# Kernel optimization log

Hardware: AMD Instinct MI355X
Metric: run time of the kernel (lower is better)

The kernel has to match this reference:

```python
import jax, jax.numpy as jnp
import numpy as np

EPS = 1e-5
H, W, C, NCLS = 8, 16, 64, 8

def _bn_params(key, c):
    k1, k2, k3, k4 = jax.random.split(key, 4)
    gamma = jax.random.uniform(k1, (c,), minval=0.5, maxval=1.5)
    beta = 0.1 * jax.random.normal(k2, (c,))
    mean = 0.1 * jax.random.normal(k3, (c,))
    var = jax.random.uniform(k4, (c,), minval=0.5, maxval=1.5)
    return jnp.stack([gamma, beta, mean, var]).astype(jnp.float32)  # (4, c)

def bn2d(x, p):
    # eval-mode BatchNorm2d; p: (4, C); x: (B, C, H, W)
    g, b, m, v = p[0], p[1], p[2], p[3]
    s = g * jax.lax.rsqrt(v + EPS)
    return x * s[None, :, None, None] + (b - m * s)[None, :, None, None]

def bn1d_scalar(x, p):
    # eval-mode BatchNorm1d with 1 channel; p: (4, 1); x: (B, 1, F)
    g, b, m, v = p[0], p[1], p[2], p[3]
    s = g * jax.lax.rsqrt(v + EPS)
    return x * s + (b - m * s)

def conv_same(x, w, b):
    y = jax.lax.conv_general_dilated(x, w, (1, 1), 'SAME',
                                     dimension_numbers=('NCHW', 'OIHW', 'NCHW'))
    return y + b[None, :, None, None]

def setup_inputs() -> dict:
    key = jax.random.key(0)
    ks = jax.random.split(key, 24)
    B = 8192
    d = {}
    d['x'] = jax.random.normal(ks[0], (B, 1, H, W), dtype=jnp.float32)
    d['bn0'] = _bn_params(ks[1], 1)
    d['conv1_w'] = 0.1 * jax.random.normal(ks[2], (C, 1, 3, 3), dtype=jnp.float32)
    d['conv1_b'] = jnp.zeros((C,), jnp.float32)
    d['bn1'] = _bn_params(ks[3], C)
    d['conv2_w'] = (0.1 / np.sqrt(C)) * jax.random.normal(ks[4], (C, C, 3, 3), dtype=jnp.float32)
    d['conv2_b'] = jnp.zeros((C,), jnp.float32)
    d['bn2'] = _bn_params(ks[5], C)
    # LocallyConnected2d, kernel_size=1 -> per-pixel (out_c, in_c) weights
    d['lc3_w'] = (1.0 / np.sqrt(C)) * jax.random.normal(ks[6], (C, C, H, W), dtype=jnp.float32)
    d['bn3'] = _bn_params(ks[7], C)
    d['lc4_w'] = (1.0 / np.sqrt(C)) * jax.random.normal(ks[8], (C, C, H, W), dtype=jnp.float32)
    d['bn4'] = _bn_params(ks[9], C)
    F5 = H * W * C
    d['fc5_w'] = (1.0 / np.sqrt(F5)) * jax.random.normal(ks[10], (512, F5), dtype=jnp.float32)
    d['fc5_b'] = jnp.zeros((512,), jnp.float32)
    d['bn5'] = _bn_params(ks[11], 1)
    d['fc6_w'] = (1.0 / np.sqrt(512)) * jax.random.normal(ks[12], (512, 512), dtype=jnp.float32)
    d['fc6_b'] = jnp.zeros((512,), jnp.float32)
    d['bn6'] = _bn_params(ks[13], 1)
    d['fc7_w'] = (1.0 / np.sqrt(512)) * jax.random.normal(ks[14], (128, 512), dtype=jnp.float32)
    d['fc7_b'] = jnp.zeros((128,), jnp.float32)
    d['bn7'] = _bn_params(ks[15], 1)
    d['fc8_w'] = (1.0 / np.sqrt(128)) * jax.random.normal(ks[16], (NCLS, 128), dtype=jnp.float32)
    d['fc8_b'] = jnp.zeros((NCLS,), jnp.float32)
    return d

def reference(x, bn0, conv1_w, conv1_b, bn1, conv2_w, conv2_b, bn2,
              lc3_w, bn3, lc4_w, bn4, fc5_w, fc5_b, bn5,
              fc6_w, fc6_b, bn6, fc7_w, fc7_b, bn7, fc8_w, fc8_b):
    B = x.shape[0]
    # squeeze -> view(B, 16, 8) -> transpose(1,2) -> add channel dim
    h = jnp.swapaxes(x.reshape(B, W, H), 1, 2)[:, None]  # (B,1,H,W)
    h = bn2d(h, bn0)
    h = jax.nn.relu(bn2d(conv_same(h, conv1_w, conv1_b), bn1))
    h = jax.nn.relu(bn2d(conv_same(h, conv2_w, conv2_b), bn2))
    # locally connected, k=1: per-pixel channel mixing
    h = jax.nn.relu(bn2d(jnp.einsum('bchw,ochw->bohw', h, lc3_w), bn3))
    h = jax.nn.relu(bn2d(jnp.einsum('bchw,ochw->bohw', h, lc4_w), bn4))
    h = h.reshape(B, 1, -1)  # (B, 1, C*H*W)
    h = h @ fc5_w.T + fc5_b
    h = jax.nn.relu(bn1d_scalar(h, bn5))
    h = jax.nn.relu(bn1d_scalar(h @ fc6_w.T + fc6_b, bn6))
    h = jax.nn.relu(bn1d_scalar(h @ fc7_w.T + fc7_b, bn7))
    h = h @ fc8_w.T + fc8_b
    return h.reshape(B, NCLS)
```

## Files before the change

### kernel.cpp

```cpp
#include <hip/hip_runtime.h>
#include <hip/hip_bf16.h>

typedef unsigned short bf16_t;
typedef __attribute__((ext_vector_type(8))) short bf16x8;
typedef __attribute__((ext_vector_type(8))) unsigned short u16x8;
typedef __attribute__((ext_vector_type(4))) float f32x4;

#if defined(__has_builtin)
#if __has_builtin(__builtin_amdgcn_global_load_lds)
#define HAS_GLL 1
#endif
#endif

__device__ __forceinline__ float b2f(bf16_t u) {
    return __uint_as_float(((unsigned int)u) << 16);
}
__device__ __forceinline__ bf16_t f2b(float f) {
    unsigned int x = __float_as_uint(f);
    unsigned int r = x + 0x7fffu + ((x >> 16) & 1u);
    return (bf16_t)(r >> 16);
}
__device__ __forceinline__ unsigned int pk2(float a, float b) {
    __hip_bfloat162 t = __float22bfloat162_rn(make_float2(a, b));
    return *(unsigned int*)&t;
}
__device__ __forceinline__ float ldf(const void* p, int i, int isf) {
    return isf ? ((const float*)p)[i] : b2f(((const bf16_t*)p)[i]);
}
__device__ __forceinline__ u16x8 ld8(const void* p, size_t off, int isf) {
    u16x8 o;
    if (isf) {
        const float* f = (const float*)p + off;
        #pragma unroll
        for (int j = 0; j < 8; j++) o[j] = f2b(f[j]);
    } else {
        o = *(const u16x8*)((const bf16_t*)p + off);
    }
    return o;
}

__device__ __forceinline__ void stg16(const bf16_t* g, bf16_t* l) {
#ifdef HAS_GLL
    __builtin_amdgcn_global_load_lds(
        (const __attribute__((address_space(1))) unsigned int*)g,
        (__attribute__((address_space(3))) unsigned int*)l,
        16, 0, 0);
#else
    *(uint4*)l = *(const uint4*)g;
#endif
}

__device__ __forceinline__ int detect_isf(const void* xraw) {
    const unsigned int* w = (const unsigned int*)xraw;
    unsigned int u = w[threadIdx.x & 63];
    float a = fabsf(__uint_as_float(u << 16));
    int g = (a >= 0.0009765625f && a <= 16.0f) ? 1 : 0;
    unsigned long long m = __ballot(g);
    return (__builtin_popcountll(m) >= 32) ? 0 : 1;
}

#define OFF_S0T0 0
#define OFF_W1   16
#define OFF_S1   592
#define OFF_H1   656
#define OFF_S2   720
#define OFF_H2   784
#define OFF_S3   848
#define OFF_H3   912
#define OFF_S4   976
#define OFF_H4   1040
#define OFF_SC5  1104
#define OFF_H5   1112
#define OFF_SC6  1624
#define OFF_H6   1632
#define OFF_SC7  2144
#define OFF_H7   2152
#define OFF_W8   2280
#define OFF_B8   3304
#define OFF_FLAG 4032

__global__ __launch_bounds__(256) void setup_fold_kernel(
    const void* __restrict__ x,
    const void* __restrict__ w2, const void* __restrict__ w3,
    const void* __restrict__ w4, const void* __restrict__ w5,
    const void* __restrict__ w6, const void* __restrict__ w7,
    bf16_t* __restrict__ w2p, bf16_t* __restrict__ w3p,
    bf16_t* __restrict__ w4p, bf16_t* __restrict__ w5p,
    bf16_t* __restrict__ w6b, bf16_t* __restrict__ w7b,
    const void* __restrict__ bn0p, const void* __restrict__ w1,
    const void* __restrict__ b1, const void* __restrict__ bn1p,
    const void* __restrict__ b2c, const void* __restrict__ bn2p,
    const void* __restrict__ bn3p, const void* __restrict__ bn4p,
    const void* __restrict__ b5, const void* __restrict__ bn5p,
    const void* __restrict__ b6, const void* __restrict__ bn6p,
    const void* __restrict__ b7, const void* __restrict__ bn7p,
    const void* __restrict__ w8, const void* __restrict__ b8,
    float* __restrict__ prm, bf16_t* __restrict__ c1, int Bf)
{
    const int t  = threadIdx.x;
    const int bb = blockIdx.x;
    const int isf = detect_isf(x);

    if (bb >= 945) {
        const int b0 = (bb - 945) * 4;
        __shared__ float xn[720];
        __shared__ float w1s[576];

        float s0, t0;
        {
            float g = ldf(bn0p, 0, isf), be = ldf(bn0p, 1, isf);
            float m = ldf(bn0p, 2, isf), v = ldf(bn0p, 3, isf);
            s0 = g * rsqrtf(v + 1e-5f); t0 = be - m * s0;
        }
        for (int i = t; i < 576; i += 256) w1s[i] = ldf(w1, i, isf);
        for (int i = t; i < 720; i += 256) {
            int s = i / 180, r = i - s * 180;
            int row = r / 18, col = r - row * 18;
            float v = 0.f;
            if (row >= 1 && row <= 8 && col >= 1 && col <= 16)
                v = s0 * ldf(x, (b0 + s) * 128 + (col - 1) * 8 + (row - 1), isf) + t0;
            xn[i] = v;
        }

        const int oc0 = (t & 7) * 8;
        const int pg  = t >> 3;

        float s1[8], h1[8];
        #pragma unroll
        for (int j = 0; j < 8; j++) {
            const int ch = oc0 + j;
            float g = ldf(bn1p, ch, isf), be = ldf(bn1p, 64 + ch, isf);
            float m = ldf(bn1p, 128 + ch, isf), v = ldf(bn1p, 192 + ch, isf);
            s1[j] = g * rsqrtf(v + 1e-5f);
            h1[j] = s1[j] * ldf(b1, ch, isf) + (be - m * s1[j]);
        }
        __syncthreads();

        for (int s = 0; s < 4; s++) {
            const int b = b0 + s;
            const float* xs = xn + s * 180;
            #pragma unroll
            for (int m = 0; m < 4; m++) {
                int p = pg + 32 * m;
                int h = p >> 4, w = p & 15;
                float r[9];
                #pragma unroll
                for (int dh = 0; dh < 3; dh++)
                    #pragma unroll
                    for (int dw = 0; dw < 3; dw++)
                        r[dh * 3 + dw] = xs[(h + dh) * 18 + (w + dw)];
                u16x8 o;
                #pragma unroll
                for (int j = 0; j < 8; j++) {
                    float acc = 0.f;
                    #pragma unroll
                    for (int k = 0; k < 9; k++) acc += r[k] * w1s[(oc0 + j) * 9 + k];
                    o[j] = f2b(fmaxf(s1[j] * acc + h1[j], 0.f));
                }
                *(u16x8*)(c1 + (size_t)p * Bf * 64 + (size_t)b * 64 + oc0) = o;
            }
        }
        return;
    }

    if (bb < 512) {
        __shared__ unsigned short ls[128 * 66];
        const int nr = bb;
        const size_t so = (size_t)nr * 8192;
        #pragma unroll
        for (int k = 0; k < 4; k++) {
            const int e0 = (t + k * 256) * 8;
            u16x8 v = ld8(w5, so + e0, isf);
            const int c = e0 >> 7, p0 = e0 & 127;
            #pragma unroll
            for (int j = 0; j < 8; j++) ls[(p0 + j) * 66 + c] = v[j];
        }
        __syncthreads();
        #pragma unroll
        for (int k = 0; k < 4; k++) {
            const int d0 = (t + k * 256) * 8;
            const int p = d0 >> 6, c0 = d0 & 63;
            u16x8 o;
            #pragma unroll
            for (int j = 0; j < 8; j++) o[j] = ls[p * 66 + c0 + j];
            *(u16x8*)(w5p + so + d0) = o;
        }
        return;
    }
    if (bb < 640) {
        __shared__ unsigned short ls[128 * 66];
        const int oc = (bb - 512) & 63;
        const void* src = (bb < 576) ? w3 : w4;
        bf16_t*    dst = (bb < 576) ? w3p : w4p;
        const size_t so = (size_t)oc * 8192;
        #pragma unroll
        for (int k = 0; k < 4; k++) {
            const int e0 = (t + k * 256) * 8;
            u16x8 v = ld8(src, so + e0, isf);
            const int ic = e0 >> 7, p0 = e0 & 127;
            #pragma unroll
            for (int j = 0; j < 8; j++) ls[(p0 + j) * 66 + ic] = v[j];
        }
        __syncthreads();
        #pragma unroll
        for (int k = 0; k < 4; k++) {
            const int d0 = (t + k * 256) * 8;
            const int p = d0 >> 6, ic0 = d0 & 63;
            u16x8 o;
            #pragma unroll
            for (int j = 0; j < 8; j++) o[j] = ls[p * 66 + ic0 + j];
            *(u16x8*)(dst + (size_t)p * 4096 + oc * 64 + ic0) = o;
        }
        return;
    }
    if (bb < 768) {
        const int i0 = ((bb - 640) * 256 + t) * 8;
        *(u16x8*)(w6b + i0) = ld8(w6, i0, isf);
        return;
    }
    if (bb < 800) {
        const int i0 = ((bb - 768) * 256 + t) * 8;
        *(u16x8*)(w7b + i0) = ld8(w7, i0, isf);
        return;
    }
    if (bb < 944) {
        const int i = (bb - 800) * 256 + t;
        int oc = i / 576, r = i - oc * 576;
        int tap = r >> 6, ic = r & 63;
        w2p[i] = f2b(ldf(w2, oc * 576 + ic * 9 + tap, isf));
        return;
    }

    if (t == 0) prm[OFF_FLAG] = isf ? 1.0f : 0.0f;

    if (t == 0) {
        float g = ldf(bn0p, 0, isf), be = ldf(bn0p, 1, isf);
        float m = ldf(bn0p, 2, isf), v = ldf(bn0p, 3, isf);
        float s = g * rsqrtf(v + 1e-5f);
        prm[OFF_S0T0] = s; prm[OFF_S0T0 + 1] = be - m * s;
    }
    for (int i = t; i < 576; i += 256) prm[OFF_W1 + i] = ldf(w1, i, isf);

    if (t < 64) {
        {
            float g = ldf(bn1p, t, isf), be = ldf(bn1p, 64 + t, isf);
            float m = ldf(bn1p, 128 + t, isf), v = ldf(bn1p, 192 + t, isf);
            float s = g * rsqrtf(v + 1e-5f);
            prm[OFF_S1 + t] = s;
            prm[OFF_H1 + t] = s * ldf(b1, t, isf) + (be - m * s);
        }
        {
            float g = ldf(bn2p, t, isf), be = ldf(bn2p, 64 + t, isf);
            float m = ldf(bn2p, 128 + t, isf), v = ldf(bn2p, 192 + t, isf);
            float s = g * rsqrtf(v + 1e-5f);
            prm[OFF_S2 + t] = s;
            prm[OFF_H2 + t] = s * ldf(b2c, t, isf) + (be - m * s);
        }
        {
            float g = ldf(bn3p, t, isf), be = ldf(bn3p, 64 + t, isf);
            float m = ldf(bn3p, 128 + t, isf), v = ldf(bn3p, 192 + t, isf);
            float s = g * rsqrtf(v + 1e-5f);
            prm[OFF_S3 + t] = s;
            prm[OFF_H3 + t] = be - m * s;
        }
        {
            float g = ldf(bn4p, t, isf), be = ldf(bn4p, 64 + t, isf);
            float m = ldf(bn4p, 128 + t, isf), v = ldf(bn4p, 192 + t, isf);
            float s = g * rsqrtf(v + 1e-5f);
            prm[OFF_S4 + t] = s;
            prm[OFF_H4 + t] = be - m * s;
        }
    }
    {
        float g = ldf(bn5p, 0, isf), be = ldf(bn5p, 1, isf);
        float m = ldf(bn5p, 2, isf), v = ldf(bn5p, 3, isf);
        float s = g * rsqrtf(v + 1e-5f);
        if (t == 0) prm[OFF_SC5] = s;
        for (int i = t; i < 512; i += 256)
            prm[OFF_H5 + i] = s * ldf(b5, i, isf) + (be - m * s);
    }
    {
        float g = ldf(bn6p, 0, isf), be = ldf(bn6p, 1, isf);
        float m = ldf(bn6p, 2, isf), v = ldf(bn6p, 3, isf);
        float s = g * rsqrtf(v + 1e-5f);
        if (t == 0) prm[OFF_SC6] = s;
        for (int i = t; i < 512; i += 256)
            prm[OFF_H6 + i] = s * ldf(b6, i, isf) + (be - m * s);
    }
    {
        float g = ldf(bn7p, 0, isf), be = ldf(bn7p, 1, isf);
        float m = ldf(bn7p, 2, isf), v = ldf(bn7p, 3, isf);
        float s = g * rsqrtf(v + 1e-5f);
        if (t == 0) prm[OFF_SC7] = s;
        if (t < 128) prm[OFF_H7 + t] = s * ldf(b7, t, isf) + (be - m * s);
    }
    for (int i = t; i < 1024; i += 256) prm[OFF_W8 + i] = ldf(w8, i, isf);
    if (t < 8) prm[OFF_B8 + t] = ldf(b8, t, isf);
}

__global__ __launch_bounds__(256) void conv1_kernel(
    const void* __restrict__ x, const float* __restrict__ prm,
    bf16_t* __restrict__ c1, int Bc, int c0)
{
    __shared__ float xn[720];
    __shared__ float w1s[576];

    const int t = threadIdx.x;
    const int b0 = blockIdx.x * 4;
    const int isf = prm[OFF_FLAG] > 0.5f;
    const float s0 = prm[OFF_S0T0], t0 = prm[OFF_S0T0 + 1];

    for (int i = t; i < 576; i += 256) w1s[i] = prm[OFF_W1 + i];
    for (int i = t; i < 720; i += 256) {
        int s = i / 180, r = i - s * 180;
        int row = r / 18, col = r - row * 18;
        float v = 0.f;
        if (row >= 1 && row <= 8 && col >= 1 && col <= 16)
            v = s0 * ldf(x, (c0 + b0 + s) * 128 + (col - 1) * 8 + (row - 1), isf) + t0;
        xn[i] = v;
    }

    const int oc0 = (t & 7) * 8;
    const int pg  = t >> 3;

    float s1[8], h1[8];
    #pragma unroll
    for (int j = 0; j < 8; j++) {
        s1[j] = prm[OFF_S1 + oc0 + j];
        h1[j] = prm[OFF_H1 + oc0 + j];
    }
    __syncthreads();

    for (int s = 0; s < 4; s++) {
        const int b = b0 + s;
        const float* xs = xn + s * 180;
        #pragma unroll
        for (int m = 0; m < 4; m++) {
            int p = pg + 32 * m;
            int h = p >> 4, w = p & 15;
            float r[9];
            #pragma unroll
            for (int dh = 0; dh < 3; dh++)
                #pragma unroll
                for (int dw = 0; dw < 3; dw++)
                    r[dh * 3 + dw] = xs[(h + dh) * 18 + (w + dw)];
            u16x8 o;
            #pragma unroll
            for (int j = 0; j < 8; j++) {
                float acc = 0.f;
                #pragma unroll
                for (int k = 0; k < 9; k++) acc += r[k] * w1s[(oc0 + j) * 9 + k];
                o[j] = f2b(fmaxf(s1[j] * acc + h1[j], 0.f));
            }
            *(u16x8*)(c1 + (size_t)p * Bc * 64 + (size_t)b * 64 + oc0) = o;
        }
    }
}

__global__ __launch_bounds__(256) void fused_mfma_kernel(
    const bf16_t* __restrict__ c1, const bf16_t* __restrict__ w2p,
    const bf16_t* __restrict__ w3p, const bf16_t* __restrict__ w4p,
    const float* __restrict__ prm, bf16_t* __restrict__ bufA, int Bc)
{
    __shared__ bf16_t sm[20480];
    const int t    = threadIdx.x;
    const int lane = t & 63;
    const int wv   = t >> 6;

    int btile, p;
    {
        const int nbx = gridDim.x;
        const int id = blockIdx.x + nbx * blockIdx.y;
        if ((nbx & 7) == 0) {
            const int xcd = id & 7;
            const int k   = id >> 3;
            p     = k & 127;
            btile = xcd + 8 * (k >> 7);
        } else {
            btile = blockIdx.x; p = blockIdx.y;
        }
    }
    const int m0 = btile * 256;
    const int h  = p >> 4, w = p & 15;

    const int fr = lane & 15;
    const int fg = lane >> 4;
    const int swz4 = (fr >> 1) & 3;

    const int gS    = (t & 3) ^ ((t >> 3) & 3);
    const int rA    = t >> 2;
    const int coff0 = rA * 64 + gS * 8;
    const int w2off = rA * 576 + gS * 8;

    u16x8 wr3[2], wr4[2];
    {
        const bf16_t* w3b = w3p + (size_t)p * 4096 + coff0;
        const bf16_t* w4b = w4p + (size_t)p * 4096 + coff0;
        wr3[0] = *(const u16x8*)(w3b);
        wr3[1] = *(const u16x8*)(w3b + 32);
        wr4[0] = *(const u16x8*)(w4b);
        wr4[1] = *(const u16x8*)(w4b + 32);
    }

    f32x4 acc[4][4];
    #pragma unroll
    for (int i = 0; i < 4; i++)
        #pragma unroll
        for (int j = 0; j < 4; j++)
            acc[i][j] = (f32x4){0.f, 0.f, 0.f, 0.f};

    const bf16_t* c1b = c1 + (size_t)m0 * 64 + coff0;
    const size_t planeStride = (size_t)Bc * 64;

    {
        if (h > 0 && w > 0) {
            const bf16_t* ab = c1b + (size_t)((h - 1) * 16 + (w - 1)) * planeStride;
            #pragma unroll
            for (int u = 0; u < 4; u++)
                stg16(ab + u * 4096, sm + t * 8 + u * 2048);
            stg16(w2p + w2off, sm + 16384 + t * 8);
        }
    }
    #pragma unroll
    for (int s = 0; s < 18; s++) {
        const int cur = s & 1;
        __syncthreads();
        if (s + 1 < 18) {
            const int s1  = s + 1;
            const int tap = s1 >> 1;
            const int dh = tap / 3 - 1, dw = tap % 3 - 1;
            const int hh = h + dh, ww = w + dw;
            if (hh >= 0 && hh < 8 && ww >= 0 && ww < 16) {
                const int nb  = cur ^ 1;
                const int ic0 = (s1 & 1) * 32;
                const bf16_t* ab = c1b + (size_t)(hh * 16 + ww) * planeStride + ic0;
                #pragma unroll
                for (int u = 0; u < 4; u++)
                    stg16(ab + u * 4096, sm + nb * 8192 + t * 8 + u * 2048);
                stg16(w2p + w2off + tap * 64 + ic0, sm + 16384 + nb * 2048 + t * 8);
            }
        }
        {
            const int tap = s >> 1;
            const int dh = tap / 3 - 1, dw = tap % 3 - 1;
            const int hh = h + dh, ww = w + dw;
            if (hh >= 0 && hh < 8 && ww >= 0 && ww < 16) {
                const bf16_t* Ab = sm + cur * 8192;
                const bf16_t* Bb = sm + 16384 + cur * 2048;
                bf16x8 hf[4], wf[4];
                #pragma unroll
                for (int j = 0; j < 4; j++)
                    hf[j] = *(const bf16x8*)(Ab + ((wv * 64 + j * 16 + fr) * 4 + (fg ^ swz4)) * 8);
                #pragma unroll
                for (int i = 0; i < 4; i++)
                    wf[i] = *(const bf16x8*)(Bb + ((i * 16 + fr) * 4 + (fg ^ swz4)) * 8);
                #pragma unroll
                for (int i = 0; i < 4; i++)
                    #pragma unroll
                    for (int j = 0; j < 4; j++)
                        acc[i][j] = __builtin_amdgcn_mfma_f32_16x16x32_bf16(
                            wf[i], hf[j], acc[i][j], 0, 0, 0);
            }
        }
    }
    __syncthreads();

#define EPILOGUE(SOFF, HOFF)                                                  \
    _Pragma("unroll")                                                         \
    for (int i = 0; i < 4; i++) {                                             \
        const int oc0e = i * 16 + fg * 4;                                     \
        const float4 sv = *(const float4*)(prm + (SOFF) + oc0e);              \
        const float4 hv = *(const float4*)(prm + (HOFF) + oc0e);              \
        _Pragma("unroll")                                                     \
        for (int j = 0; j < 4; j++) {                                         \
            const int bi = wv * 64 + j * 16 + fr;                             \
            float v0 = fmaxf(sv.x * acc[i][j][0] + hv.x, 0.f);                \
            float v1 = fmaxf(sv.y * acc[i][j][1] + hv.y, 0.f);                \
            float v2 = fmaxf(sv.z * acc[i][j][2] + hv.z, 0.f);                \
            float v3 = fmaxf(sv.w * acc[i][j][3] + hv.w, 0.f);                \
            uint2 pk; pk.x = pk2(v0, v1); pk.y = pk2(v2, v3);                 \
            *(uint2*)(sm + bi * 72 + oc0e) = pk;                              \
        }                                                                     \
    }

    EPILOGUE(OFF_S2, OFF_H2)
    *(u16x8*)(sm + 18432 + t * 8) = wr3[0];
    __syncthreads();

    #pragma unroll
    for (int i = 0; i < 4; i++)
        #pragma unroll
        for (int j = 0; j < 4; j++)
            acc[i][j] = (f32x4){0.f, 0.f, 0.f, 0.f};

    #pragma unroll
    for (int ks = 0; ks < 2; ks++) {
        if (ks == 1) {
            __syncthreads();
            *(u16x8*)(sm + 18432 + t * 8) = wr3[1];
            __syncthreads();
        }
        bf16x8 hf[4], wf[4];
        #pragma unroll
        for (int j = 0; j < 4; j++)
            hf[j] = *(const bf16x8*)(sm + (wv * 64 + j * 16 + fr) * 72 + ks * 32 + fg * 8);
        #pragma unroll
        for (int i = 0; i < 4; i++)
            wf[i] = *(const bf16x8*)(sm + 18432 + ((i * 16 + fr) * 4 + (fg ^ swz4)) * 8);
        #pragma unroll
        for (int i = 0; i < 4; i++)
            #pragma unroll
            for (int j = 0; j < 4; j++)
                acc[i][j] = __builtin_amdgcn_mfma_f32_16x16x32_bf16(
                    wf[i], hf[j], acc[i][j], 0, 0, 0);
    }

    EPILOGUE(OFF_S3, OFF_H3)
    __syncthreads();
    *(u16x8*)(sm + 18432 + t * 8) = wr4[0];
    __syncthreads();

    #pragma unroll
    for (int i = 0; i < 4; i++)
        #pragma unroll
        for (int j = 0; j < 4; j++)
            acc[i][j] = (f32x4){0.f, 0.f, 0.f, 0.f};

    #pragma unroll
    for (int ks = 0; ks < 2; ks++) {
        if (ks == 1) {
            __syncthreads();
            *(u16x8*)(sm + 18432 + t * 8) = wr4[1];
            __syncthreads();
        }
        bf16x8 hf[4], wf[4];
        #pragma unroll
        for (int j = 0; j < 4; j++)
            hf[j] = *(const bf16x8*)(sm + (wv * 64 + j * 16 + fr) * 72 + ks * 32 + fg * 8);
        #pragma unroll
        for (int i = 0; i < 4; i++)
            wf[i] = *(const bf16x8*)(sm + 18432 + ((i * 16 + fr) * 4 + (fg ^ swz4)) * 8);
        #pragma unroll
        for (int i = 0; i < 4; i++)
            #pragma unroll
            for (int j = 0; j < 4; j++)
                acc[i][j] = __builtin_amdgcn_mfma_f32_16x16x32_bf16(
                    wf[i], hf[j], acc[i][j], 0, 0, 0);
    }

    EPILOGUE(OFF_S4, OFF_H4)
#undef EPILOGUE
    __syncthreads();

    const int orow = t >> 3, wc0 = (t & 7) * 8;
    #pragma unroll
    for (int pass = 0; pass < 8; pass++) {
        const int row = orow + pass * 32;
        *(uint4*)(bufA + (size_t)(m0 + row) * 8192 + p * 64 + wc0) =
            *(const uint4*)(sm + row * 72 + wc0);
    }
}

__global__ __launch_bounds__(256) void gemm_mfma(
    const bf16_t* __restrict__ A, const bf16_t* __restrict__ W,
    const float* __restrict__ prm, int sc_off, int sh_off,
    bf16_t* __restrict__ out, int K, int N)
{
    __shared__ bf16_t sm[24576];
    const int t    = threadIdx.x;
    const int lane = t & 63;
    const int wv   = t >> 6;
    const int wr   = wv >> 1, wc = wv & 1;

    int bm, bn;
    {
        const int nx = gridDim.x, ny = gridDim.y;
        const int id = blockIdx.x + nx * blockIdx.y;
        if ((nx & 7) == 0) {
            const int xcd = id & 7;
            const int k   = id >> 3;
            const int pl  = k / ny;
            bn = k - pl * ny;
            bm = xcd + 8 * pl;
        } else {
            bm = blockIdx.x; bn = blockIdx.y;
        }
    }
    const int m0 = bm * 128, n0 = bn * 64;

    const int fr = lane & 15;
    const int fg = lane >> 4;
    const int swz8 = fr & 7;

    const bf16_t* srcA[4]; bf16_t* dstA[4];
    #pragma unroll
    for (int u = 0; u < 4; u++) {
        const int c = t + 256 * u;
        const int row = c >> 3;
        const int g = (c & 7) ^ (row & 7);
        srcA[u] = A + (size_t)(m0 + row) * K + g * 8;
        dstA[u] = sm + c * 8;
    }
    const bf16_t* srcB[2]; bf16_t* dstB[2];
    #pragma unroll
    for (int u = 0; u < 2; u++) {
        const int c = t + 256 * u;
        const int row = c >> 3;
        const int g = (c & 7) ^ (row & 7);
        srcB[u] = W + (size_t)(n0 + row) * K + g * 8;
        dstB[u] = sm + 16384 + c * 8;
    }

    f32x4 acc[4][2];
    #pragma unroll
    for (int i = 0; i < 4; i++)
        #pragma unroll
        for (int j = 0; j < 2; j++)
            acc[i][j] = (f32x4){0.f, 0.f, 0.f, 0.f};

    const int KS = K >> 6;

    #pragma unroll
    for (int u = 0; u < 4; u++) stg16(srcA[u], dstA[u]);
    #pragma unroll
    for (int u = 0; u < 2; u++) stg16(srcB[u], dstB[u]);

    for (int ks = 0; ks < KS; ks++) {
        const int cur = ks & 1;
        __syncthreads();
        if (ks + 1 < KS) {
            const int nb = cur ^ 1;
            const int kk = (ks + 1) << 6;
            #pragma unroll
            for (int u = 0; u < 4; u++) stg16(srcA[u] + kk, dstA[u] + nb * 8192);
            #pragma unroll
            for (int u = 0; u < 2; u++) stg16(srcB[u] + kk, dstB[u] + nb * 4096);
        }
        const bf16_t* Ab = sm + cur * 8192;
        const bf16_t* Bb = sm + 16384 + cur * 4096;
        bf16x8 af[4][2], bf2[2][2];
        #pragma unroll
        for (int i = 0; i < 4; i++)
            #pragma unroll
            for (int hh = 0; hh < 2; hh++) {
                const int r = wr * 64 + i * 16 + fr;
                const int g = hh * 4 + fg;
                af[i][hh] = *(const bf16x8*)(Ab + (r * 8 + (g ^ swz8)) * 8);
            }
        #pragma unroll
        for (int j = 0; j < 2; j++)
            #pragma unroll
            for (int hh = 0; hh < 2; hh++) {
                const int r = wc * 32 + j * 16 + fr;
                const int g = hh * 4 + fg;
                bf2[j][hh] = *(const bf16x8*)(Bb + (r * 8 + (g ^ swz8)) * 8);
            }
        #pragma unroll
        for (int hh = 0; hh < 2; hh++)
            #pragma unroll
            for (int i = 0; i < 4; i++)
                #pragma unroll
                for (int j = 0; j < 2; j++)
                    acc[i][j] = __builtin_amdgcn_mfma_f32_16x16x32_bf16(
                        af[i][hh], bf2[j][hh], acc[i][j], 0, 0, 0);
    }

    const float s    = prm[sc_off];
    const int   orow = fg * 4;
    const int   ocol = fr;
    #pragma unroll
    for (int j = 0; j < 2; j++) {
        const int n  = n0 + wc * 32 + j * 16 + ocol;
        const float sh = prm[sh_off + n];
        #pragma unroll
        for (int i = 0; i < 4; i++) {
            const int mb = m0 + wr * 64 + i * 16 + orow;
            #pragma unroll
            for (int r = 0; r < 4; r++) {
                float v = fmaxf(s * acc[i][j][r] + sh, 0.f);
                out[(size_t)(mb + r) * N + n] = f2b(v);
            }
        }
    }
}

__global__ __launch_bounds__(256) void fc78_kernel(
    const bf16_t* __restrict__ A, const bf16_t* __restrict__ W,
    const float* __restrict__ prm, void* __restrict__ out, int c0)
{
    __shared__ bf16_t sm[32768];
    const int t    = threadIdx.x;
    const int lane = t & 63;
    const int wv   = t >> 6;
    const int wr   = wv >> 1, wc = wv & 1;
    const int m0   = blockIdx.x * 128;
    const int K    = 512;

    const int fr = lane & 15;
    const int fg = lane >> 4;
    const int swz8 = fr & 7;

    const bf16_t* srcA[4]; bf16_t* dstA[4];
    #pragma unroll
    for (int u = 0; u < 4; u++) {
        const int c = t + 256 * u;
        const int row = c >> 3;
        const int g = (c & 7) ^ (row & 7);
        srcA[u] = A + (size_t)(m0 + row) * K + g * 8;
        dstA[u] = sm + c * 8;
    }
    const bf16_t* srcB[4]; bf16_t* dstB[4];
    #pragma unroll
    for (int u = 0; u < 4; u++) {
        const int c = t + 256 * u;
        const int row = c >> 3;
        const int g = (c & 7) ^ (row & 7);
        srcB[u] = W + (size_t)row * K + g * 8;
        dstB[u] = sm + 16384 + c * 8;
    }

    f32x4 acc[4][4];
    #pragma unroll
    for (int i = 0; i < 4; i++)
        #pragma unroll
        for (int j = 0; j < 4; j++)
            acc[i][j] = (f32x4){0.f, 0.f, 0.f, 0.f};

    const int KS = 8;

    #pragma unroll
    for (int u = 0; u < 4; u++) stg16(srcA[u], dstA[u]);
    #pragma unroll
    for (int u = 0; u < 4; u++) stg16(srcB[u], dstB[u]);

    for (int ks = 0; ks < KS; ks++) {
        const int cur = ks & 1;
        __syncthreads();
        if (ks + 1 < KS) {
            const int nb = cur ^ 1;
            const int kk = (ks + 1) << 6;
            #pragma unroll
            for (int u = 0; u < 4; u++) stg16(srcA[u] + kk, dstA[u] + nb * 8192);
            #pragma unroll
            for (int u = 0; u < 4; u++) stg16(srcB[u] + kk, dstB[u] + nb * 8192);
        }
        const bf16_t* Ab = sm + cur * 8192;
        const bf16_t* Bb = sm + 16384 + cur * 8192;
        bf16x8 af[4][2], bf2[4][2];
        #pragma unroll
        for (int i = 0; i < 4; i++)
            #pragma unroll
            for (int hh = 0; hh < 2; hh++) {
                const int r = wr * 64 + i * 16 + fr;
                const int g = hh * 4 + fg;
                af[i][hh] = *(const bf16x8*)(Ab + (r * 8 + (g ^ swz8)) * 8);
            }
        #pragma unroll
        for (int j = 0; j < 4; j++)
            #pragma unroll
            for (int hh = 0; hh < 2; hh++) {
                const int r = wc * 64 + j * 16 + fr;
                const int g = hh * 4 + fg;
                bf2[j][hh] = *(const bf16x8*)(Bb + (r * 8 + (g ^ swz8)) * 8);
            }
        #pragma unroll
        for (int hh = 0; hh < 2; hh++)
            #pragma unroll
            for (int i = 0; i < 4; i++)
                #pragma unroll
                for (int j = 0; j < 4; j++)
                    acc[i][j] = __builtin_amdgcn_mfma_f32_16x16x32_bf16(
                        af[i][hh], bf2[j][hh], acc[i][j], 0, 0, 0);
    }

    __syncthreads();
    float* w8s = (float*)(sm + 16640);
    for (int i = t; i < 1024; i += 256) w8s[i] = prm[OFF_W8 + i];

    const float s = prm[OFF_SC7];
    #pragma unroll
    for (int j = 0; j < 4; j++) {
        const int n  = wc * 64 + j * 16 + fr;
        const float sh = prm[OFF_H7 + n];
        #pragma unroll
        for (int i = 0; i < 4; i++) {
            const int row0 = wr * 64 + i * 16 + fg * 4;
            #pragma unroll
            for (int r = 0; r < 4; r++) {
                float v = fmaxf(s * acc[i][j][r] + sh, 0.f);
                sm[(row0 + r) * 130 + n] = f2b(v);
            }
        }
    }
    __syncthreads();

    const int isf = prm[OFF_FLAG] > 0.5f;
    const int r   = t & 127;
    const int n4  = (t >> 7) * 4;
    float a4[4];
    #pragma unroll
    for (int q = 0; q < 4; q++) a4[q] = prm[OFF_B8 + n4 + q];
    for (int k = 0; k < 128; k++) {
        const float hv = b2f(sm[r * 130 + k]);
        #pragma unroll
        for (int q = 0; q < 4; q++) a4[q] += hv * w8s[(n4 + q) * 128 + k];
    }
    const size_t ob = (size_t)(c0 + m0 + r) * 8 + n4;
    if (isf) {
        float4 o4 = make_float4(a4[0], a4[1], a4[2], a4[3]);
        *(float4*)((float*)out + ob) = o4;
    } else {
        uint2 pk; pk.x = pk2(a4[0], a4[1]); pk.y = pk2(a4[2], a4[3]);
        *(uint2*)((bf16_t*)out + ob) = pk;
    }
}

extern "C" void kernel_launch(void* const* d_in, const int* in_sizes, int n_in,
                              void* d_out, int out_size, void* d_ws, size_t ws_size,
                              hipStream_t stream)
{
    const void* x    = d_in[0];
    const void* bn0p = d_in[1];
    const void* w1   = d_in[2];
    const void* b1   = d_in[3];
    const void* bn1p = d_in[4];
    const void* w2   = d_in[5];
    const void* b2c  = d_in[6];
    const void* bn2p = d_in[7];
    const void* w3   = d_in[8];
    const void* bn3p = d_in[9];
    const void* w4   = d_in[10];
    const void* bn4p = d_in[11];
    const void* w5   = d_in[12];
    const void* b5   = d_in[13];
    const void* bn5p = d_in[14];
    const void* w6   = d_in[15];
    const void* b6   = d_in[16];
    const void* bn6p = d_in[17];
    const void* w7   = d_in[18];
    const void* b7   = d_in[19];
    const void* bn7p = d_in[20];
    const void* w8   = d_in[21];
    const void* b8   = d_in[22];

    char* base = (char*)d_ws;
    float*  prm = (float*)(base + 0);
    bf16_t* w2p = (bf16_t*)(base + 16384);
    bf16_t* w3p = (bf16_t*)(base + 90112);
    bf16_t* w4p = (bf16_t*)(base + 1138688);
    bf16_t* w5p = (bf16_t*)(base + 2187264);
    bf16_t* w6b = (bf16_t*)(base + 10575872);
    bf16_t* w7b = (bf16_t*)(base + 11100160);
    char*   acts = base + 11231232;

    const int B = 8192;
    const size_t FIXED = 11231232ull;

    const size_t NEED_1PASS = FIXED + (size_t)B * 16384ull + (size_t)B * 18688ull;
    const size_t NEED_2PASS = FIXED + 4096ull * 16384ull + (size_t)B * 18688ull;

    if (ws_size >= NEED_2PASS) {
        const int Bf = (ws_size >= NEED_1PASS) ? 8192 : 4096;

        bf16_t* c1   = (bf16_t*)acts;
        bf16_t* bufA = c1 + (size_t)Bf * 8192;
        bf16_t* bufC = bufA + (size_t)B * 8192;
        bf16_t* bufD = bufC + (size_t)B * 512;

        const int extra = (Bf == 8192) ? Bf / 4 : 0;
        setup_fold_kernel<<<945 + extra, 256, 0, stream>>>(
            x, w2, w3, w4, w5, w6, w7, w2p, w3p, w4p, w5p, w6b, w7b,
            bn0p, w1, b1, bn1p, b2c, bn2p, bn3p, bn4p,
            b5, bn5p, b6, bn6p, b7, bn7p, w8, b8, prm, c1, Bf);

        for (int c0 = 0; c0 < B; c0 += Bf) {
            if (extra == 0)
                conv1_kernel<<<Bf / 4, 256, 0, stream>>>(x, prm, c1, Bf, c0);
            fused_mfma_kernel<<<dim3(Bf / 256, 128), 256, 0, stream>>>(
                c1, w2p, w3p, w4p, prm, bufA + (size_t)c0 * 8192, Bf);
        }
        gemm_mfma<<<dim3(B / 128, 8), 256, 0, stream>>>(
            bufA, w5p, prm, OFF_SC5, OFF_H5, bufC, 8192, 512);
        gemm_mfma<<<dim3(B / 128, 8), 256, 0, stream>>>(
            bufC, w6b, prm, OFF_SC6, OFF_H6, bufD, 512, 512);
        fc78_kernel<<<B / 128, 256, 0, stream>>>(bufD, w7b, prm, d_out, 0);
    } else {
        size_t avail = (ws_size > FIXED) ? (ws_size - FIXED) : 0;
        int Bc = 8192;
        while (Bc > 256 && (size_t)Bc * 35072ull > avail) Bc >>= 1;

        bf16_t* c1   = (bf16_t*)acts;
        bf16_t* bufA = c1 + (size_t)Bc * 8192;
        bf16_t* bufC = bufA + (size_t)Bc * 8192;
        bf16_t* bufD = bufC + (size_t)Bc * 512;

        setup_fold_kernel<<<945, 256, 0, stream>>>(
            x, w2, w3, w4, w5, w6, w7, w2p, w3p, w4p, w5p, w6b, w7b,
            bn0p, w1, b1, bn1p, b2c, bn2p, bn3p, bn4p,
            b5, bn5p, b6, bn6p, b7, bn7p, w8, b8, prm, c1, Bc);

        for (int c0 = 0; c0 < B; c0 += Bc) {
            conv1_kernel<<<Bc / 4, 256, 0, stream>>>(x, prm, c1, Bc, c0);
            fused_mfma_kernel<<<dim3(Bc / 256, 128), 256, 0, stream>>>(
                c1, w2p, w3p, w4p, prm, bufA, Bc);
            gemm_mfma<<<dim3(Bc / 128, 8), 256, 0, stream>>>(
                bufA, w5p, prm, OFF_SC5, OFF_H5, bufC, 8192, 512);
            gemm_mfma<<<dim3(Bc / 128, 8), 256, 0, stream>>>(
                bufC, w6b, prm, OFF_SC6, OFF_H6, bufD, 512, 512);
            fc78_kernel<<<Bc / 128, 256, 0, stream>>>(bufD, w7b, prm, d_out, c0);
        }
    }
}
```

Measured before the change: 390.1 us.

## Deepen conv2 MFMA pipeline to four LDS buffers with prefetch distance two

The conv2 stage loop goes from double to quadruple buffering in LDS and issues global-to-LDS loads two steps ahead. A manual vmcnt wait lets the previous stage's loads stay in flight across the barrier, replacing the plain __syncthreads. The aim is to hide more global memory latency behind the MFMA work. In exchange, LDS use doubles to 80KB per block, which may cut occupancy, and the hand-written vmcnt counts must match the number of outstanding loads.

```diff
diff --git a/kernel.cpp b/kernel.cpp
--- a/kernel.cpp
+++ b/kernel.cpp
@@ -362,7 +362,7 @@
     const bf16_t* __restrict__ w3p, const bf16_t* __restrict__ w4p,
     const float* __restrict__ prm, bf16_t* __restrict__ bufA, int Bc)
 {
-    __shared__ bf16_t sm[20480];
+    __shared__ bf16_t sm[40960];
     const int t    = threadIdx.x;
     const int lane = t & 63;
     const int wv   = t >> 6;
@@ -412,57 +412,52 @@
     const bf16_t* c1b = c1 + (size_t)m0 * 64 + coff0;
     const size_t planeStride = (size_t)Bc * 64;
 
-    {
-        if (h > 0 && w > 0) {
-            const bf16_t* ab = c1b + (size_t)((h - 1) * 16 + (w - 1)) * planeStride;
-            #pragma unroll
-            for (int u = 0; u < 4; u++)
-                stg16(ab + u * 4096, sm + t * 8 + u * 2048);
-            stg16(w2p + w2off, sm + 16384 + t * 8);
-        }
-    }
+#define PV(k) (h + ((k) >> 1) / 3 - 1 >= 0 && h + ((k) >> 1) / 3 - 1 < 8 && \
+               w + ((k) >> 1) % 3 - 1 >= 0 && w + ((k) >> 1) % 3 - 1 < 16)
+#define STAGE(k) do {                                                         \
+    const int tap_ = (k) >> 1, icq_ = ((k) & 1) * 32;                         \
+    const int hh_ = h + tap_ / 3 - 1, ww_ = w + tap_ % 3 - 1;                 \
+    const int nb_ = (k) & 3;                                                  \
+    const bf16_t* ab_ = c1b + (size_t)(hh_ * 16 + ww_) * planeStride + icq_;  \
+    _Pragma("unroll")                                                         \
+    for (int u_ = 0; u_ < 4; u_++)                                            \
+        stg16(ab_ + u_ * 4096, sm + nb_ * 8192 + t * 8 + u_ * 2048);          \
+    stg16(w2p + w2off + tap_ * 64 + icq_, sm + 32768 + nb_ * 2048 + t * 8);   \
+} while (0)
+
+    if (PV(0)) STAGE(0);
+    if (PV(1)) STAGE(1);
+
     #pragma unroll
     for (int s = 0; s < 18; s++) {
-        const int cur = s & 1;
-        __syncthreads();
-        if (s + 1 < 18) {
-            const int s1  = s + 1;
-            const int tap = s1 >> 1;
-            const int dh = tap / 3 - 1, dw = tap % 3 - 1;
-            const int hh = h + dh, ww = w + dw;
-            if (hh >= 0 && hh < 8 && ww >= 0 && ww < 16) {
-                const int nb  = cur ^ 1;
-                const int ic0 = (s1 & 1) * 32;
-                const bf16_t* ab = c1b + (size_t)(hh * 16 + ww) * planeStride + ic0;
-                #pragma unroll
-                for (int u = 0; u < 4; u++)
-                    stg16(ab + u * 4096, sm + nb * 8192 + t * 8 + u * 2048);
-                stg16(w2p + w2off + tap * 64 + ic0, sm + 16384 + nb * 2048 + t * 8);
-            }
-        }
-        {
-            const int tap = s >> 1;
-            const int dh = tap / 3 - 1, dw = tap % 3 - 1;
-            const int hh = h + dh, ww = w + dw;
-            if (hh >= 0 && hh < 8 && ww >= 0 && ww < 16) {
-                const bf16_t* Ab = sm + cur * 8192;
-                const bf16_t* Bb = sm + 16384 + cur * 2048;
-                bf16x8 hf[4], wf[4];
+        if (s < 17 && PV(s + 1))
+            asm volatile("s_waitcnt vmcnt(5)" ::: "memory");
+        else
+            asm volatile("s_waitcnt vmcnt(0)" ::: "memory");
+        __builtin_amdgcn_sched_barrier(0);
+        __builtin_amdgcn_s_barrier();
+        __builtin_amdgcn_sched_barrier(0);
+        if (s + 2 < 18 && PV(s + 2)) STAGE(s + 2);
+        if (PV(s)) {
+            const bf16_t* Ab = sm + (s & 3) * 8192;
+            const bf16_t* Bb = sm + 32768 + (s & 3) * 2048;
+            bf16x8 hf[4], wf[4];
+            #pragma unroll
+            for (int j = 0; j < 4; j++)
+                hf[j] = *(const bf16x8*)(Ab + ((wv * 64 + j * 16 + fr) * 4 + (fg ^ swz4)) * 8);
+            #pragma unroll
+            for (int i = 0; i < 4; i++)
+                wf[i] = *(const bf16x8*)(Bb + ((i * 16 + fr) * 4 + (fg ^ swz4)) * 8);
+            #pragma unroll
+            for (int i = 0; i < 4; i++)
                 #pragma unroll
                 for (int j = 0; j < 4; j++)
-                    hf[j] = *(const bf16x8*)(Ab + ((wv * 64 + j * 16 + fr) * 4 + (fg ^ swz4)) * 8);
-                #pragma unroll
-                for (int i = 0; i < 4; i++)
-                    wf[i] = *(const bf16x8*)(Bb + ((i * 16 + fr) * 4 + (fg ^ swz4)) * 8);
-                #pragma unroll
-                for (int i = 0; i < 4; i++)
-                    #pragma unroll
-                    for (int j = 0; j < 4; j++)
-                        acc[i][j] = __builtin_amdgcn_mfma_f32_16x16x32_bf16(
-                            wf[i], hf[j], acc[i][j], 0, 0, 0);
-            }
-        }
-    }
+                    acc[i][j] = __builtin_amdgcn_mfma_f32_16x16x32_bf16(
+                        wf[i], hf[j], acc[i][j], 0, 0, 0);
+        }
+    }
+#undef STAGE
+#undef PV
     __syncthreads();
 
 #define EPILOGUE(SOFF, HOFF)                                                  \
```

New measurement: 388.3 us. No clear change (-0.5%).

## Split fc5 GEMM along K into two halves with separate reduction kernel

Applied to the files above, without the earlier changes.

Replaces the single fc5 GEMM launch (M=8192, N=512, K=8192) with a split-K kernel that gives each of two z-slices half of K. Each slice writes fp32 partial sums into a scratch buffer that reuses the conv1 activation area. A new elementwise kernel sums the two partials, applies the folded BN scale/shift and ReLU, and packs the result to bf16. The aim is to double the number of blocks and add XCD-aware block remapping for better cache locality. The cost is an extra launch plus a 32 MB fp32 write and read-back, and a large-K GEMM with 512 blocks on this GPU may already keep the CUs busy.

```diff
diff --git a/kernel.cpp b/kernel.cpp
--- a/kernel.cpp
+++ b/kernel.cpp
@@ -682,6 +682,147 @@
             }
         }
     }
+}
+
+__global__ __launch_bounds__(256) void gemm_splitk(
+    const bf16_t* __restrict__ A, const bf16_t* __restrict__ W,
+    float* __restrict__ part, int K, int N)
+{
+    __shared__ bf16_t sm[24576];
+    const int t    = threadIdx.x;
+    const int lane = t & 63;
+    const int wv   = t >> 6;
+    const int wr   = wv >> 1, wc = wv & 1;
+    const int M    = gridDim.x * 128;
+    const int kb   = blockIdx.z * (K >> 1);
+
+    int bm, bn;
+    {
+        const int nx = gridDim.x, ny = gridDim.y;
+        const int id = blockIdx.x + nx * blockIdx.y;
+        if ((nx & 7) == 0) {
+            const int xcd = id & 7;
+            const int k   = id >> 3;
+            const int pl  = k / ny;
+            bn = k - pl * ny;
+            bm = xcd + 8 * pl;
+        } else {
+            bm = blockIdx.x; bn = blockIdx.y;
+        }
+    }
+    const int m0 = bm * 128, n0 = bn * 64;
+
+    const int fr = lane & 15;
+    const int fg = lane >> 4;
+    const int swz8 = fr & 7;
+
+    const bf16_t* srcA[4]; bf16_t* dstA[4];
+    #pragma unroll
+    for (int u = 0; u < 4; u++) {
+        const int c = t + 256 * u;
+        const int row = c >> 3;
+        const int g = (c & 7) ^ (row & 7);
+        srcA[u] = A + (size_t)(m0 + row) * K + kb + g * 8;
+        dstA[u] = sm + c * 8;
+    }
+    const bf16_t* srcB[2]; bf16_t* dstB[2];
+    #pragma unroll
+    for (int u = 0; u < 2; u++) {
+        const int c = t + 256 * u;
+        const int row = c >> 3;
+        const int g = (c & 7) ^ (row & 7);
+        srcB[u] = W + (size_t)(n0 + row) * K + kb + g * 8;
+        dstB[u] = sm + 16384 + c * 8;
+    }
+
+    f32x4 acc[4][2];
+    #pragma unroll
+    for (int i = 0; i < 4; i++)
+        #pragma unroll
+        for (int j = 0; j < 2; j++)
+            acc[i][j] = (f32x4){0.f, 0.f, 0.f, 0.f};
+
+    const int KS = K >> 7;
+
+    #pragma unroll
+    for (int u = 0; u < 4; u++) stg16(srcA[u], dstA[u]);
+    #pragma unroll
+    for (int u = 0; u < 2; u++) stg16(srcB[u], dstB[u]);
+
+    for (int ks = 0; ks < KS; ks++) {
+        const int cur = ks & 1;
+        __syncthreads();
+        if (ks + 1 < KS) {
+            const int nb = cur ^ 1;
+            const int kk = (ks + 1) << 6;
+            #pragma unroll
+            for (int u = 0; u < 4; u++) stg16(srcA[u] + kk, dstA[u] + nb * 8192);
+            #pragma unroll
+            for (int u = 0; u < 2; u++) stg16(srcB[u] + kk, dstB[u] + nb * 4096);
+        }
+        const bf16_t* Ab = sm + cur * 8192;
+        const bf16_t* Bb = sm + 16384 + cur * 4096;
+        bf16x8 af[4][2], bf2[2][2];
+        #pragma unroll
+        for (int i = 0; i < 4; i++)
+            #pragma unroll
+            for (int hh = 0; hh < 2; hh++) {
+                const int r = wr * 64 + i * 16 + fr;
+                const int g = hh * 4 + fg;
+                af[i][hh] = *(const bf16x8*)(Ab + (r * 8 + (g ^ swz8)) * 8);
+            }
+        #pragma unroll
+        for (int j = 0; j < 2; j++)
+            #pragma unroll
+            for (int hh = 0; hh < 2; hh++) {
+                const int r = wc * 32 + j * 16 + fr;
+                const int g = hh * 4 + fg;
+                bf2[j][hh] = *(const bf16x8*)(Bb + (r * 8 + (g ^ swz8)) * 8);
+            }
+        #pragma unroll
+        for (int hh = 0; hh < 2; hh++)
+            #pragma unroll
+            for (int i = 0; i < 4; i++)
+                #pragma unroll
+                for (int j = 0; j < 2; j++)
+                    acc[i][j] = __builtin_amdgcn_mfma_f32_16x16x32_bf16(
+                        af[i][hh], bf2[j][hh], acc[i][j], 0, 0, 0);
+    }
+
+    float* pb = part + (size_t)blockIdx.z * M * N;
+    const int orow = fg * 4;
+    const int ocol = fr;
+    #pragma unroll
+    for (int j = 0; j < 2; j++) {
+        const int n = n0 + wc * 32 + j * 16 + ocol;
+        #pragma unroll
+        for (int i = 0; i < 4; i++) {
+            const int mb = m0 + wr * 64 + i * 16 + orow;
+            #pragma unroll
+            for (int r = 0; r < 4; r++)
+                pb[(size_t)(mb + r) * N + n] = acc[i][j][r];
+        }
+    }
+}
+
+__global__ __launch_bounds__(256) void reduce5_kernel(
+    const float* __restrict__ part, const float* __restrict__ prm,
+    int sc_off, int sh_off, bf16_t* __restrict__ out, int M, int N)
+{
+    const int idx = blockIdx.x * 256 + threadIdx.x;
+    const size_t i4 = (size_t)idx * 4;
+    if (i4 >= (size_t)M * N) return;
+    const int col = (int)(i4 % N);
+    const float s = prm[sc_off];
+    float4 p0 = *(const float4*)(part + i4);
+    float4 p1 = *(const float4*)(part + (size_t)M * N + i4);
+    float4 sh = *(const float4*)(prm + sh_off + col);
+    float v0 = fmaxf(s * (p0.x + p1.x) + sh.x, 0.f);
+    float v1 = fmaxf(s * (p0.y + p1.y) + sh.y, 0.f);
+    float v2 = fmaxf(s * (p0.z + p1.z) + sh.z, 0.f);
+    float v3 = fmaxf(s * (p0.w + p1.w) + sh.w, 0.f);
+    uint2 pk; pk.x = pk2(v0, v1); pk.y = pk2(v2, v3);
+    *(uint2*)(out + i4) = pk;
 }
 
 __global__ __launch_bounds__(256) void fc78_kernel(
@@ -866,6 +1007,7 @@
         bf16_t* bufA = c1 + (size_t)Bf * 8192;
         bf16_t* bufC = bufA + (size_t)B * 8192;
         bf16_t* bufD = bufC + (size_t)B * 512;
+        float*  part = (float*)c1;
 
         const int extra = (Bf == 8192) ? Bf / 4 : 0;
         setup_fold_kernel<<<945 + extra, 256, 0, stream>>>(
@@ -879,8 +1021,10 @@
             fused_mfma_kernel<<<dim3(Bf / 256, 128), 256, 0, stream>>>(
                 c1, w2p, w3p, w4p, prm, bufA + (size_t)c0 * 8192, Bf);
         }
-        gemm_mfma<<<dim3(B / 128, 8), 256, 0, stream>>>(
-            bufA, w5p, prm, OFF_SC5, OFF_H5, bufC, 8192, 512);
+        gemm_splitk<<<dim3(B / 128, 8, 2), 256, 0, stream>>>(
+            bufA, w5p, part, 8192, 512);
+        reduce5_kernel<<<B / 2, 256, 0, stream>>>(
+            part, prm, OFF_SC5, OFF_H5, bufC, B, 512);
         gemm_mfma<<<dim3(B / 128, 8), 256, 0, stream>>>(
             bufC, w6b, prm, OFF_SC6, OFF_H6, bufD, 512, 512);
         fc78_kernel<<<B / 128, 256, 0, stream>>>(bufD, w7b, prm, d_out, 0);
@@ -893,6 +1037,7 @@
         bf16_t* bufA = c1 + (size_t)Bc * 8192;
         bf16_t* bufC = bufA + (size_t)Bc * 8192;
         bf16_t* bufD = bufC + (size_t)Bc * 512;
+        float*  part = (float*)c1;
 
         setup_fold_kernel<<<945, 256, 0, stream>>>(
             x, w2, w3, w4, w5, w6, w7, w2p, w3p, w4p, w5p, w6b, w7b,
@@ -903,8 +1048,10 @@
             conv1_kernel<<<Bc / 4, 256, 0, stream>>>(x, prm, c1, Bc, c0);
             fused_mfma_kernel<<<dim3(Bc / 256, 128), 256, 0, stream>>>(
                 c1, w2p, w3p, w4p, prm, bufA, Bc);
-            gemm_mfma<<<dim3(Bc / 128, 8), 256, 0, stream>>>(
-                bufA, w5p, prm, OFF_SC5, OFF_H5, bufC, 8192, 512);
+            gemm_splitk<<<dim3(Bc / 128, 8, 2), 256, 0, stream>>>(
+                bufA, w5p, part, 8192, 512);
+            reduce5_kernel<<<Bc / 2, 256, 0, stream>>>(
+                part, prm, OFF_SC5, OFF_H5, bufC, Bc, 512);
             gemm_mfma<<<dim3(Bc / 128, 8), 256, 0, stream>>>(
                 bufC, w6b, prm, OFF_SC6, OFF_H6, bufD, 512, 512);
             fc78_kernel<<<Bc / 128, 256, 0, stream>>>(bufD, w7b, prm, d_out, c0);
```

Result: slower. 418.9 us (+7.4%).
